# Kernel optimization log

Hardware: AMD Instinct MI355X
Metric: run time of the kernel (lower is better)

The kernel has to match this reference:

```python
import jax, jax.numpy as jnp
import numpy as np

B = 65536      # batch of scenarios
IN = 16        # input_size
HL = 10        # hl_dim
NL = 3         # hl_num
T = 200        # number of time points
NPOP = 8.6e6   # population N


def setup_inputs() -> dict:
    key = jax.random.key(0)
    k0, k1, k2, k3 = jax.random.split(key, 4)
    data = jax.random.normal(k0, (B, IN), dtype=jnp.float32)
    times = jnp.arange(T, dtype=jnp.float32)
    # stacked params for the 3 param nets (gamma, beta, I0); xavier-ish scale, zero bias
    W0 = jax.random.normal(k1, (3, HL, IN), dtype=jnp.float32) * np.float32(1.0 / np.sqrt(IN))
    b0 = jnp.zeros((3, HL), jnp.float32)
    Wh = jax.random.normal(k2, (3, NL, HL, HL), dtype=jnp.float32) * np.float32(1.0 / np.sqrt(HL))
    bh = jnp.zeros((3, NL, HL), jnp.float32)
    Wo = jax.random.normal(k3, (3, 1, HL), dtype=jnp.float32) * np.float32(1.0 / np.sqrt(HL))
    bo = jnp.zeros((3, 1), jnp.float32)
    return {"data": data, "times": times, "W0": W0, "b0": b0,
            "Wh": Wh, "bh": bh, "Wo": Wo, "bo": bo}


def _param_nets(x, W0, b0, Wh, bh, Wo, bo):
    # runs the 3 tiny MLPs in parallel over leading net axis n in {gamma, beta, I0}
    h = jnp.tanh(jnp.einsum('bi,nhi->nbh', x, W0) + b0[:, None, :])
    for l in range(Wh.shape[1]):
        h = jnp.tanh(jnp.einsum('nbh,nkh->nbk', h, Wh[:, l]) + bh[:, l][:, None, :])
    out = jnp.einsum('nbh,noh->nbo', h, Wo) + bo[:, None, :]   # [3, B, 1]
    return jax.nn.softplus(out[..., 0])                        # [3, B]


def _forward_sir(data, times, W0, b0, Wh, bh, Wo, bo):
    vals = _param_nets(data, W0, b0, Wh, bh, Wo, bo)
    gamma, beta, I0 = vals[0], vals[1], vals[2]   # each [B]
    S0 = NPOP - I0
    R0 = jnp.zeros_like(S0)
    x0 = jnp.stack([S0, I0, R0], axis=1)          # [B, 3]

    def rhs(x):
        S, I = x[:, 0], x[:, 1]
        flux = beta * S * I / NPOP
        rec = gamma * I
        return jnp.stack([-flux, flux - rec, rec], axis=1)

    def step(x, dt):
        # classic RK4 over each interval between consecutive time points
        k1 = rhs(x)
        k2 = rhs(x + 0.5 * dt * k1)
        k3 = rhs(x + 0.5 * dt * k2)
        k4 = rhs(x + dt * k3)
        xn = x + (dt / 6.0) * (k1 + 2.0 * k2 + 2.0 * k3 + k4)
        return xn, xn

    dts = times[1:] - times[:-1]                  # [T-1]
    _, ys = jax.lax.scan(step, x0, dts)           # [T-1, B, 3]
    ys = jnp.concatenate([x0[None], ys], axis=0)  # [T, B, 3]
    return ys[:, :, 1:2].reshape(-1, 1)           # infected compartment, (T*B, output_size=1)


def reference(data, times, W0, b0, Wh, bh, Wo, bo):
    return _forward_sir(data, times, W0, b0, Wh, bh, Wo, bo)
```

## Files before the change

kernel.cpp:

```cpp
#include <hip/hip_runtime.h>
#include <math.h>

#define BSZ   65536
#define INP   16
#define HL    10
#define NL    3
#define TT    200
#define NPOP  8600000.0f

#define NCH8  24

__device__ __forceinline__ float fast_tanh(float x) {
    float e = exp2f(x * 2.8853900817779268f);
    return 1.0f - 2.0f * __builtin_amdgcn_rcpf(e + 1.0f);
}

__device__ __forceinline__ float fast_softplus(float x) {
    float t = exp2f(-fabsf(x) * 1.4426950408889634f);
    return fmaxf(x, 0.0f) + 0.6931471805599453f * log2f(1.0f + t);
}

__global__ __launch_bounds__(256) void mlp_kernel(
    const float* __restrict__ data,
    const float* __restrict__ W0,  const float* __restrict__ b0,
    const float* __restrict__ Wh,  const float* __restrict__ bh,
    const float* __restrict__ Wo,  const float* __restrict__ bo,
    float* __restrict__ vals)
{
    const int n   = blockIdx.y;
    const int tid = threadIdx.x;

    __shared__ float sW0[HL * INP];
    __shared__ float sb0[HL];
    __shared__ float sWh[NL * HL * HL];
    __shared__ float sbh[NL * HL];
    __shared__ float sWo[HL];
    __shared__ float sbo;

    for (int i = tid; i < HL * INP;      i += 256) sW0[i] = W0[n * HL * INP + i];
    for (int i = tid; i < HL;            i += 256) sb0[i] = b0[n * HL + i];
    for (int i = tid; i < NL * HL * HL;  i += 256) sWh[i] = Wh[n * NL * HL * HL + i];
    for (int i = tid; i < NL * HL;       i += 256) sbh[i] = bh[n * NL * HL + i];
    for (int i = tid; i < HL;            i += 256) sWo[i] = Wo[n * HL + i];
    if (tid == 0) sbo = bo[n];
    __syncthreads();

    const int b = blockIdx.x * 256 + tid;

    float x[INP];
    const float4* xin = reinterpret_cast<const float4*>(data + (size_t)b * INP);
    #pragma unroll
    for (int q = 0; q < INP / 4; ++q) {
        float4 v = xin[q];
        x[q * 4 + 0] = v.x; x[q * 4 + 1] = v.y;
        x[q * 4 + 2] = v.z; x[q * 4 + 3] = v.w;
    }

    float h[HL];
    #pragma unroll
    for (int k = 0; k < HL; ++k) {
        float acc = sb0[k];
        #pragma unroll
        for (int i = 0; i < INP; ++i)
            acc = fmaf(x[i], sW0[k * INP + i], acc);
        h[k] = fast_tanh(acc);
    }
    #pragma unroll
    for (int l = 0; l < NL; ++l) {
        float h2[HL];
        #pragma unroll
        for (int k = 0; k < HL; ++k) {
            float acc = sbh[l * HL + k];
            #pragma unroll
            for (int i = 0; i < HL; ++i)
                acc = fmaf(h[i], sWh[(l * HL + k) * HL + i], acc);
            h2[k] = fast_tanh(acc);
        }
        #pragma unroll
        for (int k = 0; k < HL; ++k) h[k] = h2[k];
    }
    float acc = sbo;
    #pragma unroll
    for (int i = 0; i < HL; ++i)
        acc = fmaf(h[i], sWo[i], acc);

    vals[(size_t)n * BSZ + b] = fast_softplus(acc);
}

__global__ __launch_bounds__(64, 1) void sir_kernel(
    const float* __restrict__ vals,
    const float* __restrict__ times,
    float* __restrict__ out)
{
    const int tid = threadIdx.x;
    const int b   = blockIdx.x * 64 + tid;

    const float g    = vals[b];
    const float beta = vals[BSZ + b];
    const float I0   = vals[2 * BSZ + b];

    __shared__ float sdt[208];
    for (int i = tid; i < 208; i += 64)
        sdt[i] = (i < TT - 1) ? (times[i + 1] - times[i]) : 0.0f;
    __syncthreads();

    const float bn = beta * (1.0f / NPOP);
    float I = I0;
    float P = bn * (NPOP - I0);

    {
        unsigned v0 = (unsigned)b * 4u;
        asm volatile("global_store_dword %0, %1, %2"
                     :: "v"(v0), "v"(I), "s"(out) : "memory");
    }

    auto step = [&](float dt) {
        const float hdt = 0.5f * dt;
        const float hb  = bn * hdt;
        const float db  = bn * dt;
        const float c6  = dt * (1.0f / 6.0f);
        const float cb  = bn * c6;
        float f1 = P * I;
        float m1 = fmaf(-g, I, f1);
        float aP = fmaf(-hb, f1, P);
        float aI = fmaf(hdt, m1, I);
        float f2 = aP * aI;
        float m2 = fmaf(-g, aI, f2);
        float bP = fmaf(-hb, f2, P);
        float bI = fmaf(hdt, m2, I);
        float f3 = bP * bI;
        float m3 = fmaf(-g, bI, f3);
        float cP = fmaf(-db, f3, P);
        float cI = fmaf(dt, m3, I);
        float f4 = cP * cI;
        float m4 = fmaf(-g, cI, f4);
        float s1 = m1 + m4;
        float s2 = m2 + m3;
        float u1 = f1 + f4;
        float u2 = f2 + f3;
        I = fmaf(c6, fmaf(2.0f, s2, s1), I);
        P = fmaf(-cb, fmaf(2.0f, u2, u1), P);
    };

    const float4* sdt4 = reinterpret_cast<const float4*>(sdt);

    float4 da = sdt4[0];
    float4 db4 = sdt4[1];
    float* op = out + BSZ;

    #pragma unroll 1
    for (int gch = 0; gch < NCH8; ++gch) {
        float4 na = sdt4[2 * gch + 2];
        float4 nb = sdt4[2 * gch + 3];
        __builtin_amdgcn_sched_barrier(0);

        float ic0, ic1, ic2, ic3, ic4, ic5, ic6, ic7;
        step(da.x);  ic0 = I; op[b          ] = ic0;
        step(da.y);  ic1 = I; op[b + 1 * BSZ] = ic1;
        step(da.z);  ic2 = I; op[b + 2 * BSZ] = ic2;
        step(da.w);  ic3 = I; op[b + 3 * BSZ] = ic3;
        step(db4.x); ic4 = I; op[b + 4 * BSZ] = ic4;
        step(db4.y); ic5 = I; op[b + 5 * BSZ] = ic5;
        step(db4.z); ic6 = I; op[b + 6 * BSZ] = ic6;
        step(db4.w); ic7 = I; op[b + 7 * BSZ] = ic7;

        asm volatile("" :: "v"(ic0), "v"(ic1), "v"(ic2), "v"(ic3),
                           "v"(ic4), "v"(ic5), "v"(ic6), "v"(ic7));

        da = na; db4 = nb;
        op += 8 * BSZ;
    }

    {
        float d0 = sdt[192], d1 = sdt[193], d2 = sdt[194], d3 = sdt[195];
        float d4 = sdt[196], d5 = sdt[197], d6 = sdt[198];
        float ic0, ic1, ic2, ic3, ic4, ic5, ic6;
        step(d0); ic0 = I; op[b          ] = ic0;
        step(d1); ic1 = I; op[b + 1 * BSZ] = ic1;
        step(d2); ic2 = I; op[b + 2 * BSZ] = ic2;
        step(d3); ic3 = I; op[b + 3 * BSZ] = ic3;
        step(d4); ic4 = I; op[b + 4 * BSZ] = ic4;
        step(d5); ic5 = I; op[b + 5 * BSZ] = ic5;
        step(d6); ic6 = I; op[b + 6 * BSZ] = ic6;
        asm volatile("" :: "v"(ic0), "v"(ic1), "v"(ic2), "v"(ic3),
                           "v"(ic4), "v"(ic5), "v"(ic6));
    }
}

extern "C" void kernel_launch(void* const* d_in, const int* in_sizes, int n_in,
                              void* d_out, int out_size, void* d_ws, size_t ws_size,
                              hipStream_t stream) {
    const float* data  = (const float*)d_in[0];
    const float* times = (const float*)d_in[1];
    const float* W0    = (const float*)d_in[2];
    const float* b0    = (const float*)d_in[3];
    const float* Wh    = (const float*)d_in[4];
    const float* bh    = (const float*)d_in[5];
    const float* Wo    = (const float*)d_in[6];
    const float* bo    = (const float*)d_in[7];
    float* out  = (float*)d_out;
    float* vals = (float*)d_ws;

    dim3 gridA(BSZ / 256, 3);
    mlp_kernel<<<gridA, 256, 0, stream>>>(data, W0, b0, Wh, bh, Wo, bo, vals);
    sir_kernel<<<BSZ / 64, 64, 0, stream>>>(vals, times, out);
}
```

Measured before the change: 30.72 us.

## Stage SIR outputs in LDS and emit transposed dwordx4 global stores

The SIR kernel now writes each of 16 timesteps' I values into a shared-memory buffer. Each lane then reads back a 4-wide slice and issues 128-bit global stores through hand-placed inline asm with precomputed offsets, in place of per-step scalar 32-bit stores. The aim is fewer store instructions and fewer outstanding memory operations per wave. In exchange it adds LDS round trips, hand-managed vmcnt waits and many live VGPRs holding store data and addresses, and the correctness of the tail handling for 199 steps rests on the manual offset arithmetic.

Result: no change. 30.33 us (-1.3%).

```diff
diff --git a/kernel.cpp b/kernel.cpp
--- a/kernel.cpp
+++ b/kernel.cpp
@@ -7,8 +7,10 @@
 #define NL    3
 #define TT    200
 #define NPOP  8600000.0f
-
-#define NCH8  24
+#define ROWB  262144u
+#define STEPB (64u * ROWB)
+
+typedef float f32x4 __attribute__((ext_vector_type(4)));
 
 __device__ __forceinline__ float fast_tanh(float x) {
     float e = exp2f(x * 2.8853900817779268f);
@@ -87,19 +89,26 @@
     vals[(size_t)n * BSZ + b] = fast_softplus(acc);
 }
 
+#define ST4(VOFF, VAL) \
+    asm volatile("global_store_dwordx4 %0, %1, %2" \
+                 :: "v"(VOFF), "v"(VAL), "s"(out) : "memory")
+
 __global__ __launch_bounds__(64, 1) void sir_kernel(
     const float* __restrict__ vals,
     const float* __restrict__ times,
     float* __restrict__ out)
 {
-    const int tid = threadIdx.x;
-    const int b   = blockIdx.x * 64 + tid;
+    const int tid  = threadIdx.x;
+    const int b    = blockIdx.x * 64 + tid;
+    const int lrow = tid >> 4;
+    const int lcol = tid & 15;
 
     const float g    = vals[b];
     const float beta = vals[BSZ + b];
     const float I0   = vals[2 * BSZ + b];
 
     __shared__ float sdt[208];
+    __shared__ float sbuf[16][68];
     for (int i = tid; i < 208; i += 64)
         sdt[i] = (i < TT - 1) ? (times[i + 1] - times[i]) : 0.0f;
     __syncthreads();
@@ -144,46 +153,89 @@
 
     const float4* sdt4 = reinterpret_cast<const float4*>(sdt);
 
-    float4 da = sdt4[0];
-    float4 db4 = sdt4[1];
-    float* op = out + BSZ;
+    const unsigned colb = ((unsigned)blockIdx.x * 64u + 4u * (unsigned)lcol) * 4u;
+    unsigned vo00, vo01, vo02, vo03, vo10, vo11, vo12, vo13;
+    unsigned vo20, vo21, vo22, vo23, vo30, vo31, vo32, vo33;
+    #define VINIT(S, Q) (unsigned)(16 * (S) + 4 * (Q) + lrow + 1) * ROWB + colb
+    vo00 = VINIT(0,0); vo01 = VINIT(0,1); vo02 = VINIT(0,2); vo03 = VINIT(0,3);
+    vo10 = VINIT(1,0); vo11 = VINIT(1,1); vo12 = VINIT(1,2); vo13 = VINIT(1,3);
+    vo20 = VINIT(2,0); vo21 = VINIT(2,1); vo22 = VINIT(2,2); vo23 = VINIT(2,3);
+    vo30 = VINIT(3,0); vo31 = VINIT(3,1); vo32 = VINIT(3,2); vo33 = VINIT(3,3);
+
+    f32x4 sd00 = 0, sd01 = 0, sd02 = 0, sd03 = 0;
+    f32x4 sd10 = 0, sd11 = 0, sd12 = 0, sd13 = 0;
+    f32x4 sd20 = 0, sd21 = 0, sd22 = 0, sd23 = 0;
+    f32x4 sd30 = 0, sd31 = 0, sd32 = 0, sd33 = 0;
+
+    float4 d0 = sdt4[0], d1 = sdt4[1], d2 = sdt4[2], d3 = sdt4[3];
+
+    auto chunk16 = [&](int nextIdx) {
+        step(d0.x); sbuf[ 0][tid] = I;
+        step(d0.y); sbuf[ 1][tid] = I;
+        step(d0.z); sbuf[ 2][tid] = I;
+        step(d0.w); sbuf[ 3][tid] = I;
+        step(d1.x); sbuf[ 4][tid] = I;
+        step(d1.y); sbuf[ 5][tid] = I;
+        step(d1.z); sbuf[ 6][tid] = I;
+        step(d1.w); sbuf[ 7][tid] = I;
+        step(d2.x); sbuf[ 8][tid] = I;
+        step(d2.y); sbuf[ 9][tid] = I;
+        step(d2.z); sbuf[10][tid] = I;
+        step(d2.w); sbuf[11][tid] = I;
+        step(d3.x); sbuf[12][tid] = I;
+        step(d3.y); sbuf[13][tid] = I;
+        step(d3.z); sbuf[14][tid] = I;
+        step(d3.w); sbuf[15][tid] = I;
+        d0 = sdt4[nextIdx];     d1 = sdt4[nextIdx + 1];
+        d2 = sdt4[nextIdx + 2]; d3 = sdt4[nextIdx + 3];
+    };
+
+    #define LDQ(Q) (*(const f32x4*)&sbuf[4 * (Q) + lrow][4 * lcol])
+
+    #define KEEPD() asm volatile("" :: "v"(sd00), "v"(sd01), "v"(sd02), "v"(sd03), \
+        "v"(sd10), "v"(sd11), "v"(sd12), "v"(sd13), "v"(sd20), "v"(sd21), \
+        "v"(sd22), "v"(sd23), "v"(sd30), "v"(sd31), "v"(sd32), "v"(sd33))
+    #define KEEPA() asm volatile("" :: "v"(vo00), "v"(vo01), "v"(vo02), "v"(vo03), \
+        "v"(vo10), "v"(vo11), "v"(vo12), "v"(vo13), "v"(vo20), "v"(vo21), \
+        "v"(vo22), "v"(vo23), "v"(vo30), "v"(vo31), "v"(vo32), "v"(vo33))
+
+    #define BURST(S) \
+        asm volatile("s_waitcnt vmcnt(12)" ::: "memory"); \
+        KEEPD(); KEEPA(); \
+        __builtin_amdgcn_sched_barrier(0); \
+        sd##S##0 = LDQ(0); sd##S##1 = LDQ(1); \
+        sd##S##2 = LDQ(2); sd##S##3 = LDQ(3); \
+        ST4(vo##S##0, sd##S##0); ST4(vo##S##1, sd##S##1); \
+        ST4(vo##S##2, sd##S##2); ST4(vo##S##3, sd##S##3); \
+        vo##S##0 += STEPB; vo##S##1 += STEPB; \
+        vo##S##2 += STEPB; vo##S##3 += STEPB; \
+        __builtin_amdgcn_sched_barrier(0)
 
     #pragma unroll 1
-    for (int gch = 0; gch < NCH8; ++gch) {
-        float4 na = sdt4[2 * gch + 2];
-        float4 nb = sdt4[2 * gch + 3];
-        __builtin_amdgcn_sched_barrier(0);
-
-        float ic0, ic1, ic2, ic3, ic4, ic5, ic6, ic7;
-        step(da.x);  ic0 = I; op[b          ] = ic0;
-        step(da.y);  ic1 = I; op[b + 1 * BSZ] = ic1;
-        step(da.z);  ic2 = I; op[b + 2 * BSZ] = ic2;
-        step(da.w);  ic3 = I; op[b + 3 * BSZ] = ic3;
-        step(db4.x); ic4 = I; op[b + 4 * BSZ] = ic4;
-        step(db4.y); ic5 = I; op[b + 5 * BSZ] = ic5;
-        step(db4.z); ic6 = I; op[b + 6 * BSZ] = ic6;
-        step(db4.w); ic7 = I; op[b + 7 * BSZ] = ic7;
-
-        asm volatile("" :: "v"(ic0), "v"(ic1), "v"(ic2), "v"(ic3),
-                           "v"(ic4), "v"(ic5), "v"(ic6), "v"(ic7));
-
-        da = na; db4 = nb;
-        op += 8 * BSZ;
-    }
-
-    {
-        float d0 = sdt[192], d1 = sdt[193], d2 = sdt[194], d3 = sdt[195];
-        float d4 = sdt[196], d5 = sdt[197], d6 = sdt[198];
-        float ic0, ic1, ic2, ic3, ic4, ic5, ic6;
-        step(d0); ic0 = I; op[b          ] = ic0;
-        step(d1); ic1 = I; op[b + 1 * BSZ] = ic1;
-        step(d2); ic2 = I; op[b + 2 * BSZ] = ic2;
-        step(d3); ic3 = I; op[b + 3 * BSZ] = ic3;
-        step(d4); ic4 = I; op[b + 4 * BSZ] = ic4;
-        step(d5); ic5 = I; op[b + 5 * BSZ] = ic5;
-        step(d6); ic6 = I; op[b + 6 * BSZ] = ic6;
-        asm volatile("" :: "v"(ic0), "v"(ic1), "v"(ic2), "v"(ic3),
-                           "v"(ic4), "v"(ic5), "v"(ic6));
+    for (int cc = 0; cc < 3; ++cc) {
+        chunk16(4 * (4 * cc + 1)); BURST(0);
+        chunk16(4 * (4 * cc + 2)); BURST(1);
+        chunk16(4 * (4 * cc + 3)); BURST(2);
+        chunk16(4 * (4 * cc + 4)); BURST(3);
+    }
+
+    step(d0.x); sbuf[0][tid] = I;
+    step(d0.y); sbuf[1][tid] = I;
+    step(d0.z); sbuf[2][tid] = I;
+    step(d0.w); sbuf[3][tid] = I;
+    step(d1.x); sbuf[4][tid] = I;
+    step(d1.y); sbuf[5][tid] = I;
+    step(d1.z); sbuf[6][tid] = I;
+
+    asm volatile("s_waitcnt vmcnt(12)" ::: "memory");
+    KEEPD(); KEEPA();
+    __builtin_amdgcn_sched_barrier(0);
+
+    sd00 = LDQ(0);
+    ST4(vo00, sd00);
+    if (lrow < 3) {
+        sd01 = LDQ(1);
+        ST4(vo01, sd01);
     }
 }
 
```

## Split SIR kernel into compute and store wavefronts with double-buffered LDS

Applied to the files above, without the earlier changes.

Each block now runs two wavefronts. One integrates the RK4 recurrence and writes 16 timesteps at a time into a double-buffered shared-memory slab. The other wavefront drains the slab to global memory with dwordx4 stores, synchronised through s_barrier. The aim is to take the scattered per-timestep dword stores off the latency-bound compute wave and coalesce them into wider writes. The cost is barrier handshakes per chunk and a doubled block size, plus fragile hand-written barrier and waitcnt ordering.

Measured after the change: 30.28 us. Within noise of the previous version (-1.4%).

```diff
diff --git a/kernel.cpp b/kernel.cpp
--- a/kernel.cpp
+++ b/kernel.cpp
@@ -7,8 +7,9 @@
 #define NL    3
 #define TT    200
 #define NPOP  8600000.0f
-
-#define NCH8  24
+#define ROWB  262144u
+
+typedef float f32x4 __attribute__((ext_vector_type(4)));
 
 __device__ __forceinline__ float fast_tanh(float x) {
     float e = exp2f(x * 2.8853900817779268f);
@@ -87,103 +88,155 @@
     vals[(size_t)n * BSZ + b] = fast_softplus(acc);
 }
 
-__global__ __launch_bounds__(64, 1) void sir_kernel(
+#define ST4(VOFF, VAL) \
+    asm volatile("global_store_dwordx4 %0, %1, %2" \
+                 :: "v"(VOFF), "v"(VAL), "s"(out) : "memory")
+
+__global__ __launch_bounds__(128, 1) void sir_kernel(
     const float* __restrict__ vals,
     const float* __restrict__ times,
     float* __restrict__ out)
 {
     const int tid = threadIdx.x;
-    const int b   = blockIdx.x * 64 + tid;
-
-    const float g    = vals[b];
-    const float beta = vals[BSZ + b];
-    const float I0   = vals[2 * BSZ + b];
+    const int w   = tid >> 6;
+    const int l   = tid & 63;
+    const int b0  = blockIdx.x * 64;
+    const int b   = b0 + l;
 
     __shared__ float sdt[208];
-    for (int i = tid; i < 208; i += 64)
+    __shared__ float slab[2][16][68];
+
+    for (int i = tid; i < 208; i += 128)
         sdt[i] = (i < TT - 1) ? (times[i + 1] - times[i]) : 0.0f;
     __syncthreads();
 
-    const float bn = beta * (1.0f / NPOP);
-    float I = I0;
-    float P = bn * (NPOP - I0);
-
-    {
-        unsigned v0 = (unsigned)b * 4u;
-        asm volatile("global_store_dword %0, %1, %2"
-                     :: "v"(v0), "v"(I), "s"(out) : "memory");
-    }
-
-    auto step = [&](float dt) {
-        const float hdt = 0.5f * dt;
-        const float hb  = bn * hdt;
-        const float db  = bn * dt;
-        const float c6  = dt * (1.0f / 6.0f);
-        const float cb  = bn * c6;
-        float f1 = P * I;
-        float m1 = fmaf(-g, I, f1);
-        float aP = fmaf(-hb, f1, P);
-        float aI = fmaf(hdt, m1, I);
-        float f2 = aP * aI;
-        float m2 = fmaf(-g, aI, f2);
-        float bP = fmaf(-hb, f2, P);
-        float bI = fmaf(hdt, m2, I);
-        float f3 = bP * bI;
-        float m3 = fmaf(-g, bI, f3);
-        float cP = fmaf(-db, f3, P);
-        float cI = fmaf(dt, m3, I);
-        float f4 = cP * cI;
-        float m4 = fmaf(-g, cI, f4);
-        float s1 = m1 + m4;
-        float s2 = m2 + m3;
-        float u1 = f1 + f4;
-        float u2 = f2 + f3;
-        I = fmaf(c6, fmaf(2.0f, s2, s1), I);
-        P = fmaf(-cb, fmaf(2.0f, u2, u1), P);
-    };
-
     const float4* sdt4 = reinterpret_cast<const float4*>(sdt);
 
-    float4 da = sdt4[0];
-    float4 db4 = sdt4[1];
-    float* op = out + BSZ;
-
-    #pragma unroll 1
-    for (int gch = 0; gch < NCH8; ++gch) {
-        float4 na = sdt4[2 * gch + 2];
-        float4 nb = sdt4[2 * gch + 3];
+    if (w == 0) {
+        const float g    = vals[b];
+        const float beta = vals[BSZ + b];
+        const float I0v  = vals[2 * BSZ + b];
+        const float bn = beta * (1.0f / NPOP);
+        float I = I0v;
+        float P = bn * (NPOP - I0v);
+
+        auto step = [&](float dt) {
+            const float hdt = 0.5f * dt;
+            const float hb  = bn * hdt;
+            const float db  = bn * dt;
+            const float c6  = dt * (1.0f / 6.0f);
+            const float cb  = bn * c6;
+            float f1 = P * I;
+            float m1 = fmaf(-g, I, f1);
+            float aP = fmaf(-hb, f1, P);
+            float aI = fmaf(hdt, m1, I);
+            float f2 = aP * aI;
+            float m2 = fmaf(-g, aI, f2);
+            float bP = fmaf(-hb, f2, P);
+            float bI = fmaf(hdt, m2, I);
+            float f3 = bP * bI;
+            float m3 = fmaf(-g, bI, f3);
+            float cP = fmaf(-db, f3, P);
+            float cI = fmaf(dt, m3, I);
+            float f4 = cP * cI;
+            float m4 = fmaf(-g, cI, f4);
+            float s1 = m1 + m4;
+            float s2 = m2 + m3;
+            float u1 = f1 + f4;
+            float u2 = f2 + f3;
+            I = fmaf(c6, fmaf(2.0f, s2, s1), I);
+            P = fmaf(-cb, fmaf(2.0f, u2, u1), P);
+        };
+
+        float4 d0 = sdt4[0], d1 = sdt4[1], d2 = sdt4[2], d3 = sdt4[3];
+
+        #define CHUNK(BUF, NEXT) do {                                        \
+            float j0, j1, j2, j3, j4, j5, j6, j7;                            \
+            float j8, j9, j10, j11, j12, j13, j14, j15;                      \
+            step(d0.x); j0  = I;  step(d0.y); j1  = I;                       \
+            step(d0.z); j2  = I;  step(d0.w); j3  = I;                       \
+            step(d1.x); j4  = I;  step(d1.y); j5  = I;                       \
+            step(d1.z); j6  = I;  step(d1.w); j7  = I;                       \
+            step(d2.x); j8  = I;  step(d2.y); j9  = I;                       \
+            step(d2.z); j10 = I;  step(d2.w); j11 = I;                       \
+            step(d3.x); j12 = I;  step(d3.y); j13 = I;                       \
+            step(d3.z); j14 = I;  step(d3.w); j15 = I;                       \
+            slab[BUF][ 0][l] = j0;  slab[BUF][ 1][l] = j1;                   \
+            slab[BUF][ 2][l] = j2;  slab[BUF][ 3][l] = j3;                   \
+            slab[BUF][ 4][l] = j4;  slab[BUF][ 5][l] = j5;                   \
+            slab[BUF][ 6][l] = j6;  slab[BUF][ 7][l] = j7;                   \
+            slab[BUF][ 8][l] = j8;  slab[BUF][ 9][l] = j9;                   \
+            slab[BUF][10][l] = j10; slab[BUF][11][l] = j11;                  \
+            slab[BUF][12][l] = j12; slab[BUF][13][l] = j13;                  \
+            slab[BUF][14][l] = j14; slab[BUF][15][l] = j15;                  \
+            d0 = sdt4[(NEXT)];     d1 = sdt4[(NEXT) + 1];                    \
+            d2 = sdt4[(NEXT) + 2]; d3 = sdt4[(NEXT) + 3];                    \
+            asm volatile("s_waitcnt lgkmcnt(0)" ::: "memory");               \
+            __builtin_amdgcn_sched_barrier(0);                               \
+            __builtin_amdgcn_s_barrier();                                    \
+            __builtin_amdgcn_sched_barrier(0);                               \
+        } while (0)
+
+        #pragma unroll 1
+        for (int cc = 0; cc < 5; ++cc) {
+            CHUNK(0, 8 * cc + 8);
+            CHUNK(1, 8 * cc + 12);
+        }
+        CHUNK(0, 48);
+        CHUNK(1, 48);
+
+        {
+            float j0, j1, j2, j3, j4, j5, j6;
+            step(d0.x); j0 = I;  step(d0.y); j1 = I;
+            step(d0.z); j2 = I;  step(d0.w); j3 = I;
+            step(d1.x); j4 = I;  step(d1.y); j5 = I;
+            step(d1.z); j6 = I;
+            slab[0][0][l] = j0; slab[0][1][l] = j1;
+            slab[0][2][l] = j2; slab[0][3][l] = j3;
+            slab[0][4][l] = j4; slab[0][5][l] = j5;
+            slab[0][6][l] = j6;
+            asm volatile("s_waitcnt lgkmcnt(0)" ::: "memory");
+            __builtin_amdgcn_sched_barrier(0);
+            __builtin_amdgcn_s_barrier();
+        }
+    } else {
+        const int lr = l >> 4;
+        const int lc = l & 15;
+
+        out[b] = vals[2 * BSZ + b];
+
+        const unsigned cb = ((unsigned)b0 + 4u * (unsigned)lc) * 4u;
+        unsigned vo0 = (unsigned)( 1 + lr) * ROWB + cb;
+        unsigned vo1 = (unsigned)( 5 + lr) * ROWB + cb;
+        unsigned vo2 = (unsigned)( 9 + lr) * ROWB + cb;
+        unsigned vo3 = (unsigned)(13 + lr) * ROWB + cb;
+
+        #pragma unroll 1
+        for (int k = 0; k < 12; ++k) {
+            __builtin_amdgcn_s_barrier();
+            __builtin_amdgcn_sched_barrier(0);
+            asm volatile("s_waitcnt vmcnt(0)" ::: "memory");
+            const float* sb = &slab[k & 1][0][0];
+            f32x4 v0 = *(const f32x4*)(sb + (lr     ) * 68 + 4 * lc);
+            f32x4 v1 = *(const f32x4*)(sb + (lr +  4) * 68 + 4 * lc);
+            f32x4 v2 = *(const f32x4*)(sb + (lr +  8) * 68 + 4 * lc);
+            f32x4 v3 = *(const f32x4*)(sb + (lr + 12) * 68 + 4 * lc);
+            ST4(vo0, v0); ST4(vo1, v1); ST4(vo2, v2); ST4(vo3, v3);
+            vo0 += 16u * ROWB; vo1 += 16u * ROWB;
+            vo2 += 16u * ROWB; vo3 += 16u * ROWB;
+        }
+        __builtin_amdgcn_s_barrier();
         __builtin_amdgcn_sched_barrier(0);
-
-        float ic0, ic1, ic2, ic3, ic4, ic5, ic6, ic7;
-        step(da.x);  ic0 = I; op[b          ] = ic0;
-        step(da.y);  ic1 = I; op[b + 1 * BSZ] = ic1;
-        step(da.z);  ic2 = I; op[b + 2 * BSZ] = ic2;
-        step(da.w);  ic3 = I; op[b + 3 * BSZ] = ic3;
-        step(db4.x); ic4 = I; op[b + 4 * BSZ] = ic4;
-        step(db4.y); ic5 = I; op[b + 5 * BSZ] = ic5;
-        step(db4.z); ic6 = I; op[b + 6 * BSZ] = ic6;
-        step(db4.w); ic7 = I; op[b + 7 * BSZ] = ic7;
-
-        asm volatile("" :: "v"(ic0), "v"(ic1), "v"(ic2), "v"(ic3),
-                           "v"(ic4), "v"(ic5), "v"(ic6), "v"(ic7));
-
-        da = na; db4 = nb;
-        op += 8 * BSZ;
-    }
-
-    {
-        float d0 = sdt[192], d1 = sdt[193], d2 = sdt[194], d3 = sdt[195];
-        float d4 = sdt[196], d5 = sdt[197], d6 = sdt[198];
-        float ic0, ic1, ic2, ic3, ic4, ic5, ic6;
-        step(d0); ic0 = I; op[b          ] = ic0;
-        step(d1); ic1 = I; op[b + 1 * BSZ] = ic1;
-        step(d2); ic2 = I; op[b + 2 * BSZ] = ic2;
-        step(d3); ic3 = I; op[b + 3 * BSZ] = ic3;
-        step(d4); ic4 = I; op[b + 4 * BSZ] = ic4;
-        step(d5); ic5 = I; op[b + 5 * BSZ] = ic5;
-        step(d6); ic6 = I; op[b + 6 * BSZ] = ic6;
-        asm volatile("" :: "v"(ic0), "v"(ic1), "v"(ic2), "v"(ic3),
-                           "v"(ic4), "v"(ic5), "v"(ic6));
+        asm volatile("s_waitcnt vmcnt(0)" ::: "memory");
+        {
+            const float* sb = &slab[0][0][0];
+            f32x4 v0 = *(const f32x4*)(sb + (lr    ) * 68 + 4 * lc);
+            ST4(vo0, v0);
+            if (lr < 3) {
+                f32x4 v1 = *(const f32x4*)(sb + (lr + 4) * 68 + 4 * lc);
+                ST4(vo1, v1);
+            }
+        }
     }
 }
 
@@ -203,5 +256,5 @@
 
     dim3 gridA(BSZ / 256, 3);
     mlp_kernel<<<gridA, 256, 0, stream>>>(data, W0, b0, Wh, bh, Wo, bo, vals);
-    sir_kernel<<<BSZ / 64, 64, 0, stream>>>(vals, times, out);
-}
+    sir_kernel<<<BSZ / 64, 128, 0, stream>>>(vals, times, out);
+}
```

## Split RK4 time integration into boundary pass plus parallel time-segment replay

Applied to the files above, without the earlier changes.

The single sequential SIR kernel becomes two kernels. A boundary kernel integrates 175 steps with no output writes and records the state at every 25-step boundary. A segment kernel then re-integrates each of 8 segments in parallel over a 2D grid and writes the outputs. This adds parallelism along the time axis and moves the store traffic into a kernel with many more waves, at the cost of redundant compute, an extra kernel launch and workspace round-trip.

Measured after the change: 41.36 us. 1.35x slower.

```diff
diff --git a/kernel.cpp b/kernel.cpp
--- a/kernel.cpp
+++ b/kernel.cpp
@@ -7,8 +7,6 @@
 #define NL    3
 #define TT    200
 #define NPOP  8600000.0f
-
-#define NCH8  24
 
 __device__ __forceinline__ float fast_tanh(float x) {
     float e = exp2f(x * 2.8853900817779268f);
@@ -87,103 +85,113 @@
     vals[(size_t)n * BSZ + b] = fast_softplus(acc);
 }
 
-__global__ __launch_bounds__(64, 1) void sir_kernel(
+#define STEP_BODY(P, I, bn, g, dt) do {                                   \
+    const float hdt_ = 0.5f * (dt);                                       \
+    const float hb_  = (bn) * hdt_;                                       \
+    const float db_  = (bn) * (dt);                                       \
+    const float c6_  = (dt) * (1.0f / 6.0f);                              \
+    const float cb_  = (bn) * c6_;                                        \
+    float f1 = (P) * (I);                                                 \
+    float m1 = fmaf(-(g), (I), f1);                                       \
+    float aP = fmaf(-hb_, f1, (P));                                       \
+    float aI = fmaf(hdt_, m1, (I));                                       \
+    float f2 = aP * aI;                                                   \
+    float m2 = fmaf(-(g), aI, f2);                                        \
+    float bP = fmaf(-hb_, f2, (P));                                       \
+    float bI = fmaf(hdt_, m2, (I));                                       \
+    float f3 = bP * bI;                                                   \
+    float m3 = fmaf(-(g), bI, f3);                                        \
+    float cP = fmaf(-db_, f3, (P));                                       \
+    float cI = fmaf((dt), m3, (I));                                       \
+    float f4 = cP * cI;                                                   \
+    float m4 = fmaf(-(g), cI, f4);                                        \
+    float s1 = m1 + m4;                                                   \
+    float s2 = m2 + m3;                                                   \
+    float u1 = f1 + f4;                                                   \
+    float u2 = f2 + f3;                                                   \
+    (I) = fmaf(c6_, fmaf(2.0f, s2, s1), (I));                             \
+    (P) = fmaf(-cb_, fmaf(2.0f, u2, u1), (P));                            \
+} while (0)
+
+__global__ __launch_bounds__(64, 1) void boundary_kernel(
     const float* __restrict__ vals,
     const float* __restrict__ times,
+    float* __restrict__ bst)
+{
+    const int l = threadIdx.x;
+    const int b = blockIdx.x * 64 + l;
+
+    __shared__ float sdt[176];
+    __shared__ float slab[7][2][64];
+
+    for (int i = l; i < 176; i += 64)
+        sdt[i] = (i < 175) ? (times[i + 1] - times[i]) : 0.0f;
+    __syncthreads();
+
+    const float g    = vals[b];
+    const float beta = vals[BSZ + b];
+    const float I0   = vals[2 * BSZ + b];
+    const float bn   = beta * (1.0f / NPOP);
+    float I = I0;
+    float P = bn * (NPOP - I0);
+
+    #pragma unroll 1
+    for (int c = 0; c < 7; ++c) {
+        float d[25];
+        #pragma unroll
+        for (int j = 0; j < 25; ++j) d[j] = sdt[25 * c + j];
+        #pragma unroll
+        for (int j = 0; j < 25; ++j) STEP_BODY(P, I, bn, g, d[j]);
+        slab[c][0][l] = P;
+        slab[c][1][l] = I;
+    }
+    __syncthreads();
+
+    #pragma unroll
+    for (int j = 0; j < 7; ++j) {
+        bst[(size_t)j * 2 * BSZ + b]       = slab[j][0][l];
+        bst[(size_t)j * 2 * BSZ + BSZ + b] = slab[j][1][l];
+    }
+}
+
+__global__ __launch_bounds__(256) void seg_kernel(
+    const float* __restrict__ vals,
+    const float* __restrict__ times,
+    const float* __restrict__ bst,
     float* __restrict__ out)
 {
     const int tid = threadIdx.x;
-    const int b   = blockIdx.x * 64 + tid;
+    const int k   = blockIdx.y;
+    const int b   = blockIdx.x * 256 + tid;
+    const int t0  = 25 * k;
+
+    __shared__ float sdt[25];
+    if (tid < 25)
+        sdt[tid] = (t0 + tid < TT - 1) ? (times[t0 + tid + 1] - times[t0 + tid])
+                                       : 0.0f;
+    __syncthreads();
 
     const float g    = vals[b];
     const float beta = vals[BSZ + b];
-    const float I0   = vals[2 * BSZ + b];
-
-    __shared__ float sdt[208];
-    for (int i = tid; i < 208; i += 64)
-        sdt[i] = (i < TT - 1) ? (times[i + 1] - times[i]) : 0.0f;
-    __syncthreads();
-
-    const float bn = beta * (1.0f / NPOP);
-    float I = I0;
-    float P = bn * (NPOP - I0);
-
-    {
-        unsigned v0 = (unsigned)b * 4u;
-        asm volatile("global_store_dword %0, %1, %2"
-                     :: "v"(v0), "v"(I), "s"(out) : "memory");
-    }
-
-    auto step = [&](float dt) {
-        const float hdt = 0.5f * dt;
-        const float hb  = bn * hdt;
-        const float db  = bn * dt;
-        const float c6  = dt * (1.0f / 6.0f);
-        const float cb  = bn * c6;
-        float f1 = P * I;
-        float m1 = fmaf(-g, I, f1);
-        float aP = fmaf(-hb, f1, P);
-        float aI = fmaf(hdt, m1, I);
-        float f2 = aP * aI;
-        float m2 = fmaf(-g, aI, f2);
-        float bP = fmaf(-hb, f2, P);
-        float bI = fmaf(hdt, m2, I);
-        float f3 = bP * bI;
-        float m3 = fmaf(-g, bI, f3);
-        float cP = fmaf(-db, f3, P);
-        float cI = fmaf(dt, m3, I);
-        float f4 = cP * cI;
-        float m4 = fmaf(-g, cI, f4);
-        float s1 = m1 + m4;
-        float s2 = m2 + m3;
-        float u1 = f1 + f4;
-        float u2 = f2 + f3;
-        I = fmaf(c6, fmaf(2.0f, s2, s1), I);
-        P = fmaf(-cb, fmaf(2.0f, u2, u1), P);
-    };
-
-    const float4* sdt4 = reinterpret_cast<const float4*>(sdt);
-
-    float4 da = sdt4[0];
-    float4 db4 = sdt4[1];
-    float* op = out + BSZ;
+    const float bn   = beta * (1.0f / NPOP);
+
+    float P, I;
+    if (k == 0) {
+        const float I0 = vals[2 * BSZ + b];
+        I = I0;
+        P = bn * (NPOP - I0);
+        out[b] = I;
+    } else {
+        P = bst[(size_t)(k - 1) * 2 * BSZ + b];
+        I = bst[(size_t)(k - 1) * 2 * BSZ + BSZ + b];
+    }
+
+    const int ns = (k == 7) ? 24 : 25;
 
     #pragma unroll 1
-    for (int gch = 0; gch < NCH8; ++gch) {
-        float4 na = sdt4[2 * gch + 2];
-        float4 nb = sdt4[2 * gch + 3];
-        __builtin_amdgcn_sched_barrier(0);
-
-        float ic0, ic1, ic2, ic3, ic4, ic5, ic6, ic7;
-        step(da.x);  ic0 = I; op[b          ] = ic0;
-        step(da.y);  ic1 = I; op[b + 1 * BSZ] = ic1;
-        step(da.z);  ic2 = I; op[b + 2 * BSZ] = ic2;
-        step(da.w);  ic3 = I; op[b + 3 * BSZ] = ic3;
-        step(db4.x); ic4 = I; op[b + 4 * BSZ] = ic4;
-        step(db4.y); ic5 = I; op[b + 5 * BSZ] = ic5;
-        step(db4.z); ic6 = I; op[b + 6 * BSZ] = ic6;
-        step(db4.w); ic7 = I; op[b + 7 * BSZ] = ic7;
-
-        asm volatile("" :: "v"(ic0), "v"(ic1), "v"(ic2), "v"(ic3),
-                           "v"(ic4), "v"(ic5), "v"(ic6), "v"(ic7));
-
-        da = na; db4 = nb;
-        op += 8 * BSZ;
-    }
-
-    {
-        float d0 = sdt[192], d1 = sdt[193], d2 = sdt[194], d3 = sdt[195];
-        float d4 = sdt[196], d5 = sdt[197], d6 = sdt[198];
-        float ic0, ic1, ic2, ic3, ic4, ic5, ic6;
-        step(d0); ic0 = I; op[b          ] = ic0;
-        step(d1); ic1 = I; op[b + 1 * BSZ] = ic1;
-        step(d2); ic2 = I; op[b + 2 * BSZ] = ic2;
-        step(d3); ic3 = I; op[b + 3 * BSZ] = ic3;
-        step(d4); ic4 = I; op[b + 4 * BSZ] = ic4;
-        step(d5); ic5 = I; op[b + 5 * BSZ] = ic5;
-        step(d6); ic6 = I; op[b + 6 * BSZ] = ic6;
-        asm volatile("" :: "v"(ic0), "v"(ic1), "v"(ic2), "v"(ic3),
-                           "v"(ic4), "v"(ic5), "v"(ic6));
+    for (int t = 0; t < ns; ++t) {
+        STEP_BODY(P, I, bn, g, sdt[t]);
+        out[(size_t)(t0 + t + 1) * BSZ + b] = I;
     }
 }
 
@@ -200,8 +208,11 @@
     const float* bo    = (const float*)d_in[7];
     float* out  = (float*)d_out;
     float* vals = (float*)d_ws;
+    float* bst  = vals + 3 * (size_t)BSZ;
 
     dim3 gridA(BSZ / 256, 3);
     mlp_kernel<<<gridA, 256, 0, stream>>>(data, W0, b0, Wh, bh, Wo, bo, vals);
-    sir_kernel<<<BSZ / 64, 64, 0, stream>>>(vals, times, out);
-}
+    boundary_kernel<<<BSZ / 64, 64, 0, stream>>>(vals, times, bst);
+    dim3 gridC(BSZ / 256, 8);
+    seg_kernel<<<gridC, 256, 0, stream>>>(vals, times, bst, out);
+}
```
